# Optimization experiments

Measured on AMD Instinct MI355X. Metric: run time of the kernel, lower is better.

Reference implementation:

```python
import jax, jax.numpy as jnp
import numpy as np

N_NODES, N_GRAPHS, PER_GRAPH, N_EDGES = 20000, 200, 100, 320000
X_DIM, E_DIM, G_DIM = 32, 16, 32
NUM_EMB, HEADS, LAYERS = 64, 2, 3
EPS_GEN, EPS_LN = 1e-7, 1e-5


def _w(k, shape, scale=0.05):
    return (jax.random.normal(k, shape) * scale).astype(jnp.float32)


def _mlp3(x, W1, b1, W2, b2, W3, b3):
    h = jax.nn.leaky_relu(x @ W1 + b1)
    h = jax.nn.leaky_relu(h @ W2 + b2)
    return h @ W3 + b3


def _seg_sum(x, idx, n):
    return jax.ops.segment_sum(x, idx, num_segments=n)


def _seg_mean(x, idx, n):
    s = _seg_sum(x, idx, n)
    cnt = _seg_sum(jnp.ones((x.shape[0],), x.dtype), idx, n)
    return s / jnp.clip(cnt, 1.0, None)[:, None]


def _seg_softmax(logits, idx, n):
    # PyG softmax: subtract per-segment max, normalize with +1e-16
    m = jax.ops.segment_max(logits, idx, num_segments=n)
    m = jnp.where(jnp.isfinite(m), m, 0.0)
    e = jnp.exp(logits - m[idx])
    s = jax.ops.segment_sum(e, idx, num_segments=n)
    return e / (s[idx] + 1e-16)


def _graph_layernorm(x, batch, n_graphs):
    # PyG LayerNorm(mode='graph', affine=False): mean/var over all node-feature
    # entries of each graph.
    f = x.shape[-1]
    cnt = _seg_sum(jnp.ones((x.shape[0],), x.dtype), batch, n_graphs)
    norm = jnp.clip(cnt, 1.0, None) * f
    mean = _seg_sum(x.sum(-1), batch, n_graphs) / norm
    xc = x - mean[batch][:, None]
    var = _seg_sum((xc * xc).sum(-1), batch, n_graphs) / norm
    return xc / jnp.sqrt(var + EPS_LN)[batch][:, None]


def _forward(x, edge_attr, cond, edge_index, batch,
             x2h_W1, x2h_b1, x2h_W2, x2h_b2, x2h_W3, x2h_b3,
             e2h_W1, e2h_b1, e2h_W2, e2h_b2, e2h_W3, e2h_b3,
             c2h_W1, c2h_b1, c2h_W2, c2h_b2, c2h_W3, c2h_b3,
             gen_W, tr_Wq, tr_bq, tr_Wk, tr_bk, tr_Wv, tr_bv, tr_We, tr_Ws, tr_bs,
             lin_W, lin_b, ff_W1, ff_b1, ff_W2, ff_b2):
    N = x.shape[0]
    G = cond.shape[0]
    Naug = N + G
    o = _mlp3(x, x2h_W1, x2h_b1, x2h_W2, x2h_b2, x2h_W3, x2h_b3)
    e = _mlp3(edge_attr, e2h_W1, e2h_b1, e2h_W2, e2h_b2, e2h_W3, e2h_b3)
    c = _mlp3(cond, c2h_W1, c2h_b1, c2h_W2, c2h_b2, c2h_W3, c2h_b3)
    # virtual-node edges: node<->virtual node of its graph (virtual ids = N..N+G-1)
    u = jnp.arange(N, dtype=edge_index.dtype)
    v = batch.astype(edge_index.dtype) + N
    aug_ei = jnp.concatenate([edge_index, jnp.stack([u, v]), jnp.stack([v, u])], axis=1)
    e_p = jnp.zeros((2 * N, NUM_EMB), o.dtype).at[:, 0].set(1.0)
    aug_e = jnp.concatenate([e, e_p], axis=0)
    # add_self_loops(fill_value='mean'): self-loop attr = mean of incoming edge attrs
    loop_attr = _seg_mean(aug_e, aug_ei[1], Naug)
    loops = jnp.arange(Naug, dtype=edge_index.dtype)
    aug_ei = jnp.concatenate([aug_ei, jnp.stack([loops, loops])], axis=1)
    aug_e = jnp.concatenate([aug_e, loop_attr], axis=0)
    aug_batch = jnp.concatenate([batch, jnp.arange(G, dtype=batch.dtype)])
    o = jnp.concatenate([o, c], axis=0)  # [Naug, emb]
    src, dst = aug_ei[0], aug_ei[1]
    scale = 1.0 / float(np.sqrt(NUM_EMB))
    for i in range(LAYERS):
        # GENConv(aggr='add', norm=None, num_layers=1): sum(relu(x_j+e)+eps) + x, then Linear
        msg = jax.nn.relu(o[src] + aug_e) + EPS_GEN
        agg = (_seg_sum(msg, dst, Naug) + o) @ gen_W[i]
        # TransformerConv(2*emb -> emb, heads, edge_dim=emb, concat=True)
        xin = jnp.concatenate([o, agg], axis=1)  # [Naug, 2*emb]
        q = (xin @ tr_Wq[i] + tr_bq[i]).reshape(Naug, HEADS, NUM_EMB)
        k = (xin @ tr_Wk[i] + tr_bk[i]).reshape(Naug, HEADS, NUM_EMB)
        vv = (xin @ tr_Wv[i] + tr_bv[i]).reshape(Naug, HEADS, NUM_EMB)
        eh = (aug_e @ tr_We[i]).reshape(-1, HEADS, NUM_EMB)  # [E, H, C]
        kj = k[src] + eh
        alpha = _seg_softmax(jnp.einsum('ehc,ehc->eh', q[dst], kj) * scale, dst, Naug)
        tout = _seg_sum((vv[src] + eh) * alpha[..., None], dst, Naug)
        tout = tout.reshape(Naug, HEADS * NUM_EMB) + xin @ tr_Ws[i] + tr_bs[i]
        # residual + graph LayerNorm, then FFN + graph LayerNorm
        o = _graph_layernorm(o + tout @ lin_W[i] + lin_b[i], aug_batch, G)
        ff = jax.nn.leaky_relu(o @ ff_W1[i] + ff_b1[i]) @ ff_W2[i] + ff_b2[i]
        o = _graph_layernorm(o + ff, aug_batch, G)
    node_o, virt = o[:N], o[N:]
    glob = jnp.concatenate([_seg_mean(node_o, batch, G), virt, c], axis=1)
    o_final = jnp.concatenate([node_o, c[batch]], axis=1)
    return (o_final, glob)


def setup_inputs() -> dict:
    key = jax.random.key(0)
    ks = iter(jax.random.split(key, 64))
    inp = {}
    inp['x'] = jax.random.normal(next(ks), (N_NODES, X_DIM), dtype=jnp.float32)
    inp['edge_attr'] = jax.random.normal(next(ks), (N_EDGES, E_DIM), dtype=jnp.float32)
    inp['cond'] = jax.random.normal(next(ks), (N_GRAPHS, G_DIM), dtype=jnp.float32)
    src = jax.random.randint(next(ks), (N_EDGES,), 0, N_NODES)
    dst = (src // PER_GRAPH) * PER_GRAPH + jax.random.randint(next(ks), (N_EDGES,), 0, PER_GRAPH)
    inp['edge_index'] = jnp.stack([src, dst]).astype(jnp.int32)
    inp['batch'] = jnp.repeat(jnp.arange(N_GRAPHS, dtype=jnp.int32), PER_GRAPH)
    for p, nin in [('x2h', X_DIM), ('e2h', E_DIM), ('c2h', G_DIM)]:
        inp[p + '_W1'] = _w(next(ks), (nin, NUM_EMB)); inp[p + '_b1'] = _w(next(ks), (NUM_EMB,))
        inp[p + '_W2'] = _w(next(ks), (NUM_EMB, NUM_EMB)); inp[p + '_b2'] = _w(next(ks), (NUM_EMB,))
        inp[p + '_W3'] = _w(next(ks), (NUM_EMB, NUM_EMB)); inp[p + '_b3'] = _w(next(ks), (NUM_EMB,))
    HC = HEADS * NUM_EMB
    inp['gen_W'] = _w(next(ks), (LAYERS, NUM_EMB, NUM_EMB))
    inp['tr_Wq'] = _w(next(ks), (LAYERS, 2 * NUM_EMB, HC)); inp['tr_bq'] = _w(next(ks), (LAYERS, HC))
    inp['tr_Wk'] = _w(next(ks), (LAYERS, 2 * NUM_EMB, HC)); inp['tr_bk'] = _w(next(ks), (LAYERS, HC))
    inp['tr_Wv'] = _w(next(ks), (LAYERS, 2 * NUM_EMB, HC)); inp['tr_bv'] = _w(next(ks), (LAYERS, HC))
    inp['tr_We'] = _w(next(ks), (LAYERS, NUM_EMB, HC))
    inp['tr_Ws'] = _w(next(ks), (LAYERS, 2 * NUM_EMB, HC)); inp['tr_bs'] = _w(next(ks), (LAYERS, HC))
    inp['lin_W'] = _w(next(ks), (LAYERS, HC, NUM_EMB)); inp['lin_b'] = _w(next(ks), (LAYERS, NUM_EMB))
    inp['ff_W1'] = _w(next(ks), (LAYERS, NUM_EMB, 4 * NUM_EMB)); inp['ff_b1'] = _w(next(ks), (LAYERS, 4 * NUM_EMB))
    inp['ff_W2'] = _w(next(ks), (LAYERS, 4 * NUM_EMB, NUM_EMB)); inp['ff_b2'] = _w(next(ks), (LAYERS, NUM_EMB))
    return inp


def reference(x, edge_attr, cond, edge_index, batch,
              x2h_W1, x2h_b1, x2h_W2, x2h_b2, x2h_W3, x2h_b3,
              e2h_W1, e2h_b1, e2h_W2, e2h_b2, e2h_W3, e2h_b3,
              c2h_W1, c2h_b1, c2h_W2, c2h_b2, c2h_W3, c2h_b3,
              gen_W, tr_Wq, tr_bq, tr_Wk, tr_bk, tr_Wv, tr_bv, tr_We, tr_Ws, tr_bs,
              lin_W, lin_b, ff_W1, ff_b1, ff_W2, ff_b2):
    return _forward(x, edge_attr, cond, edge_index, batch,
                    x2h_W1, x2h_b1, x2h_W2, x2h_b2, x2h_W3, x2h_b3,
                    e2h_W1, e2h_b1, e2h_W2, e2h_b2, e2h_W3, e2h_b3,
                    c2h_W1, c2h_b1, c2h_W2, c2h_b2, c2h_W3, c2h_b3,
                    gen_W, tr_Wq, tr_bq, tr_Wk, tr_bk, tr_Wv, tr_bv, tr_We, tr_Ws, tr_bs,
                    lin_W, lin_b, ff_W1, ff_b1, ff_W2, ff_b2)
```

## Files before the change

kernel.cpp:

```cpp
#include <hip/hip_runtime.h>
#include <cstddef>

#define NN   20000
#define NG   200
#define NE   320000
#define NAUG 20200
#define NE2  360000
#define EAUG 380200
#define DD   64
#define HC   128

typedef float  f32x4 __attribute__((ext_vector_type(4)));
typedef short  s16x8 __attribute__((ext_vector_type(8)));

static __device__ __forceinline__ unsigned short bf16r(float f){
  unsigned u = __float_as_uint(f);
  u += 0x7FFFu + ((u >> 16) & 1u);
  return (unsigned short)(u >> 16);
}
static __device__ __forceinline__ float d4(float4 a, float4 b){
  return a.x*b.x + a.y*b.y + a.z*b.z + a.w*b.w;
}
static __device__ __forceinline__ float4 f4ab(float4 a, float s, float4 b, float t){
  return make_float4(a.x*s + b.x*t, a.y*s + b.y*t, a.z*s + b.z*t, a.w*s + b.w*t);
}
static __device__ __forceinline__ float4 f4s(float4 a, float s){
  return make_float4(a.x*s, a.y*s, a.z*s, a.w*s);
}

#define WTAB_INIT { \
  {0,0,128,128,136,128,0},{0,0,128,128,136,128,16384},{0,0,128,128,136,128,32768}, \
  {1,0,128,128,136,128,0},{1,0,128,128,136,128,16384},{1,0,128,128,136,128,32768}, \
  {2,0,128,128,136,128,0},{2,0,128,128,136,128,16384},{2,0,128,128,136,128,32768}, \
  {3,0,128,128,136,128,0},{3,0,128,128,136,128,16384},{3,0,128,128,136,128,32768}, \
  {4,0,64,64,72,64,0},{4,0,64,64,72,64,4096},{4,0,64,64,72,64,8192}, \
  {5,0,128,64,136,64,0},{5,0,128,64,136,64,8192},{5,0,128,64,136,64,16384}, \
  {6,0,64,256,72,256,0},{6,0,64,256,72,256,16384},{6,0,64,256,72,256,32768}, \
  {7,0,256,64,264,64,0},{7,0,256,64,264,64,16384},{7,0,256,64,264,64,32768}, \
  {8,1,64,64,72,128,0},{8,1,64,64,72,128,64},{8,1,64,64,72,128,8192},{8,1,64,64,72,128,8256},{8,1,64,64,72,128,16384},{8,1,64,64,72,128,16448}, \
  {8,0,64,64,72,128,0},{8,0,64,64,72,128,64},{8,0,64,64,72,128,8192},{8,0,64,64,72,128,8256},{8,0,64,64,72,128,16384},{8,0,64,64,72,128,16448}, \
  {9,0,32,64,40,64,0},{10,0,64,64,72,64,0},{11,0,64,64,72,64,0}, \
  {12,0,16,64,40,64,0},{13,0,64,64,72,64,0},{14,0,64,64,72,64,0}, \
  {15,0,32,64,40,64,0},{16,0,64,64,72,64,0},{17,0,64,64,72,64,0} }

static const int WTAB_H[45][7] = WTAB_INIT;
__device__ static const int WTAB_D[45][7] = WTAB_INIT;

struct WPtrs { const float* p[18]; };

__global__ void wconv_all_k(WPtrs wp, unsigned short* __restrict__ outbase){
  int b = blockIdx.x;
  int acc = 0; unsigned ooff = 0;
  #pragma unroll 1
  for (int j = 0; j < 45; j++){
    int e  = WTAB_D[j][3] * WTAB_D[j][4];
    int nb = (e + 255) >> 8;
    if (b < acc + nb){
      int idx = (b - acc)*256 + threadIdx.x;
      if (idx < e){
        int KP = WTAB_D[j][4];
        int n = idx / KP, k = idx % KP;
        float v = 0.f;
        if (k < WTAB_D[j][2]){
          const float* s = wp.p[WTAB_D[j][0]];
          int st = WTAB_D[j][5], so = WTAB_D[j][6];
          v = (WTAB_D[j][1] == 0) ? s[(size_t)so + (size_t)k*st + n]
                                  : s[(size_t)so + (size_t)n*st + k];
        }
        outbase[ooff + idx] = bf16r(v);
      }
      return;
    }
    acc += nb; ooff += (unsigned)e;
  }
}

template<int NT>
__launch_bounds__(256)
__global__ void gemm_mfma_k(const float* __restrict__ A, const float* __restrict__ A2,
                            int M, int K, int lda,
                            const unsigned short* __restrict__ WtG,
                            const float* __restrict__ bias, int act,
                            const float* __restrict__ res, const float* __restrict__ res2,
                            int rstride, float* __restrict__ out, int ostride){
  extern __shared__ unsigned short smem[];
  const int KC  = (K > 128) ? 128 : K;
  const int KPc = KC + 8;
  const int KP  = K + 8;
  unsigned short* Wts  = smem;
  unsigned short* Asub = smem + NT*KPc;
  const int tid = threadIdx.x;
  const int wid = tid >> 6, lane = tid & 63;
  const int lrow = lane & 15, quad = lane >> 4;
  const int m0 = blockIdx.x * 64;
  f32x4 acc[NT/16];
  #pragma unroll
  for (int t = 0; t < NT/16; t++) acc[t] = (f32x4){0.f,0.f,0.f,0.f};

  for (int k0 = 0; k0 < K; k0 += KC){
    const int wv = NT*KPc/8, wrow = KPc/8;
    for (int i = tid; i < wv; i += 256){
      int n = i / wrow, c8 = i % wrow;
      *(uint4*)&Wts[n*KPc + c8*8] = *(const uint4*)&WtG[(size_t)n*KP + k0 + c8*8];
    }
    const int av = 64*KC/4, arow = KC/4;
    for (int i = tid; i < av; i += 256){
      int r = i / arow, c4i = i % arow;
      int m = m0 + r, k = k0 + c4i*4;
      float4 v = make_float4(0.f,0.f,0.f,0.f);
      if (m < M){
        v = *(const float4*)(A + (size_t)m*lda + k);
        if (A2){ float4 w = *(const float4*)(A2 + (size_t)m*lda + k);
                 v.x += w.x; v.y += w.y; v.z += w.z; v.w += w.w; }
      }
      ushort4 s; s.x = bf16r(v.x); s.y = bf16r(v.y); s.z = bf16r(v.z); s.w = bf16r(v.w);
      *(ushort4*)&Asub[r*KPc + c4i*4] = s;
    }
    __syncthreads();
    const int ksteps = KC >> 5;
    for (int ks = 0; ks < ksteps; ks++){
      s16x8 a = *(const s16x8*)&Asub[(wid*16 + lrow)*KPc + ks*32 + quad*8];
      #pragma unroll
      for (int nt = 0; nt < NT/16; nt++){
        s16x8 b = *(const s16x8*)&Wts[(nt*16 + lrow)*KPc + ks*32 + quad*8];
        acc[nt] = __builtin_amdgcn_mfma_f32_16x16x32_bf16(a, b, acc[nt], 0, 0, 0);
      }
    }
    __syncthreads();
  }

  const int mb = m0 + wid*16 + quad*4;
  #pragma unroll
  for (int nt = 0; nt < NT/16; nt++){
    int n = nt*16 + lrow;
    #pragma unroll
    for (int r = 0; r < 4; r++){
      int m = mb + r;
      if (m < M){
        float v = acc[nt][r];
        if (bias) v += bias[n];
        if (act)  v = v > 0.f ? v : 0.01f*v;
        if (res)  v += res [(size_t)m*rstride + n];
        if (res2) v += res2[(size_t)m*rstride + n];
        out[(size_t)m*ostride + n] = v;
      }
    }
  }
}

struct PW4 { const unsigned short* w[4]; const float* b[4]; };

__launch_bounds__(256)
__global__ void qkvs4_k(const float* __restrict__ A, int M, PW4 pw,
                        float* __restrict__ out){
  __shared__ __align__(16) unsigned short Wts[128*136];
  __shared__ __align__(16) unsigned short Asub[64*136];
  const unsigned short* WtG = pw.w[blockIdx.y];
  const float* bias = pw.b[blockIdx.y];
  const int tid = threadIdx.x;
  const int wid = tid >> 6, lane = tid & 63;
  const int lrow = lane & 15, quad = lane >> 4;
  const int m0 = blockIdx.x * 64;
  for (int i = tid; i < 128*17; i += 256){
    int n = i/17, c8 = i%17;
    *(uint4*)&Wts[n*136 + c8*8] = *(const uint4*)&WtG[(size_t)n*136 + c8*8];
  }
  for (int i = tid; i < 64*32; i += 256){
    int r = i >> 5, c4 = (i & 31)*4;
    int m = m0 + r;
    float4 v = make_float4(0.f,0.f,0.f,0.f);
    if (m < M) v = *(const float4*)(A + (size_t)m*128 + c4);
    ushort4 s; s.x=bf16r(v.x); s.y=bf16r(v.y); s.z=bf16r(v.z); s.w=bf16r(v.w);
    *(ushort4*)&Asub[r*136 + c4] = s;
  }
  __syncthreads();
  f32x4 acc[8];
  #pragma unroll
  for (int t=0;t<8;t++) acc[t] = (f32x4){0.f,0.f,0.f,0.f};
  #pragma unroll
  for (int ks = 0; ks < 4; ks++){
    s16x8 a = *(const s16x8*)&Asub[(wid*16 + lrow)*136 + ks*32 + quad*8];
    #pragma unroll
    for (int nt = 0; nt < 8; nt++){
      s16x8 b = *(const s16x8*)&Wts[(nt*16 + lrow)*136 + ks*32 + quad*8];
      acc[nt] = __builtin_amdgcn_mfma_f32_16x16x32_bf16(a, b, acc[nt], 0, 0, 0);
    }
  }
  const int mb = m0 + wid*16 + quad*4;
  const int yoff = blockIdx.y*128;
  #pragma unroll
  for (int nt = 0; nt < 8; nt++){
    int n = nt*16 + lrow;
    #pragma unroll
    for (int r = 0; r < 4; r++){
      int m = mb + r;
      if (m < M) out[(size_t)m*512 + yoff + n] = acc[nt][r] + bias[n];
    }
  }
}

struct PW2 { const unsigned short* w[2]; };

__launch_bounds__(256)
__global__ void qe2_k(const float* __restrict__ qkvs, int M, PW2 pw,
                      float* __restrict__ qe){
  __shared__ __align__(16) unsigned short Wts[64*72];
  __shared__ __align__(16) unsigned short Asub[64*72];
  const unsigned short* WtG = pw.w[blockIdx.y];
  const int tid = threadIdx.x;
  const int wid = tid >> 6, lane = tid & 63;
  const int lrow = lane & 15, quad = lane >> 4;
  const int m0 = blockIdx.x * 64;
  const int yoff = blockIdx.y * 64;
  for (int i = tid; i < 64*9; i += 256){
    int n = i/9, c8 = i%9;
    *(uint4*)&Wts[n*72 + c8*8] = *(const uint4*)&WtG[(size_t)n*72 + c8*8];
  }
  for (int i = tid; i < 64*16; i += 256){
    int r = i >> 4, c4 = (i & 15)*4;
    int m = m0 + r;
    float4 v = make_float4(0.f,0.f,0.f,0.f);
    if (m < M) v = *(const float4*)(qkvs + (size_t)m*512 + yoff + c4);
    ushort4 s; s.x=bf16r(v.x); s.y=bf16r(v.y); s.z=bf16r(v.z); s.w=bf16r(v.w);
    *(ushort4*)&Asub[r*72 + c4] = s;
  }
  __syncthreads();
  f32x4 acc[4];
  #pragma unroll
  for (int t=0;t<4;t++) acc[t] = (f32x4){0.f,0.f,0.f,0.f};
  #pragma unroll
  for (int ks = 0; ks < 2; ks++){
    s16x8 a = *(const s16x8*)&Asub[(wid*16 + lrow)*72 + ks*32 + quad*8];
    #pragma unroll
    for (int nt = 0; nt < 4; nt++){
      s16x8 b = *(const s16x8*)&Wts[(nt*16 + lrow)*72 + ks*32 + quad*8];
      acc[nt] = __builtin_amdgcn_mfma_f32_16x16x32_bf16(a, b, acc[nt], 0, 0, 0);
    }
  }
  const int mb = m0 + wid*16 + quad*4;
  #pragma unroll
  for (int nt = 0; nt < 4; nt++){
    int n = nt*16 + lrow;
    #pragma unroll
    for (int r = 0; r < 4; r++){
      int m = mb + r;
      if (m < M) qe[(size_t)m*HC + yoff + n] = acc[nt][r];
    }
  }
}

__launch_bounds__(256)
__global__ void tout2_k(const float* __restrict__ wv, int M, PW2 pw,
                        const float* __restrict__ t1, const float* __restrict__ qkvs,
                        float* __restrict__ tout){
  __shared__ __align__(16) unsigned short Wts[64*72];
  __shared__ __align__(16) unsigned short Asub[64*72];
  const unsigned short* WtG = pw.w[blockIdx.y];
  const int tid = threadIdx.x;
  const int wid = tid >> 6, lane = tid & 63;
  const int lrow = lane & 15, quad = lane >> 4;
  const int m0 = blockIdx.x * 64;
  const int yoff = blockIdx.y * 64;
  for (int i = tid; i < 64*9; i += 256){
    int n = i/9, c8 = i%9;
    *(uint4*)&Wts[n*72 + c8*8] = *(const uint4*)&WtG[(size_t)n*72 + c8*8];
  }
  for (int i = tid; i < 64*16; i += 256){
    int r = i >> 4, c4 = (i & 15)*4;
    int m = m0 + r;
    float4 v = make_float4(0.f,0.f,0.f,0.f);
    if (m < M) v = *(const float4*)(wv + (size_t)m*HC + yoff + c4);
    ushort4 s; s.x=bf16r(v.x); s.y=bf16r(v.y); s.z=bf16r(v.z); s.w=bf16r(v.w);
    *(ushort4*)&Asub[r*72 + c4] = s;
  }
  __syncthreads();
  f32x4 acc[4];
  #pragma unroll
  for (int t=0;t<4;t++) acc[t] = (f32x4){0.f,0.f,0.f,0.f};
  #pragma unroll
  for (int ks = 0; ks < 2; ks++){
    s16x8 a = *(const s16x8*)&Asub[(wid*16 + lrow)*72 + ks*32 + quad*8];
    #pragma unroll
    for (int nt = 0; nt < 4; nt++){
      s16x8 b = *(const s16x8*)&Wts[(nt*16 + lrow)*72 + ks*32 + quad*8];
      acc[nt] = __builtin_amdgcn_mfma_f32_16x16x32_bf16(a, b, acc[nt], 0, 0, 0);
    }
  }
  const int mb = m0 + wid*16 + quad*4;
  #pragma unroll
  for (int nt = 0; nt < 4; nt++){
    int n = nt*16 + lrow;
    #pragma unroll
    for (int r = 0; r < 4; r++){
      int m = mb + r;
      if (m < M)
        tout[(size_t)m*HC + yoff + n] = acc[nt][r]
          + t1[(size_t)m*HC + yoff + n] + qkvs[(size_t)m*512 + 384 + yoff + n];
    }
  }
}

__launch_bounds__(256)
__global__ void mlp3_mfma_k(const float* __restrict__ X, int M, int Din,
                            const unsigned short* __restrict__ w1t,
                            const unsigned short* __restrict__ w2t,
                            const unsigned short* __restrict__ w3t,
                            const float* __restrict__ b1, const float* __restrict__ b2,
                            const float* __restrict__ b3, float* __restrict__ out){
  __shared__ __align__(16) unsigned short W1s[64*40], W2s[64*72], W3s[64*72];
  __shared__ __align__(16) unsigned short xs[64*40], hs[64*72];
  __shared__ float bsh[192];
  const int tid = threadIdx.x;
  for (int i = tid; i < 320; i += 256)  *(uint4*)&W1s[i*8] = *(const uint4*)&w1t[i*8];
  for (int i = tid; i < 576; i += 256){ *(uint4*)&W2s[i*8] = *(const uint4*)&w2t[i*8];
                                        *(uint4*)&W3s[i*8] = *(const uint4*)&w3t[i*8]; }
  if (tid < 64){ bsh[tid] = b1[tid]; bsh[64+tid] = b2[tid]; bsh[128+tid] = b3[tid]; }
  const int m0 = blockIdx.x * 64;
  for (int i = tid; i < 512; i += 256){
    int r = i >> 3, c4 = (i & 7) * 4;
    int m = m0 + r;
    float4 v = make_float4(0.f,0.f,0.f,0.f);
    if (m < M && c4 < Din) v = *(const float4*)(X + (size_t)m*Din + c4);
    ushort4 s; s.x = bf16r(v.x); s.y = bf16r(v.y); s.z = bf16r(v.z); s.w = bf16r(v.w);
    *(ushort4*)&xs[r*40 + c4] = s;
  }
  __syncthreads();
  const int wid = tid >> 6, lane = tid & 63;
  const int lrow = lane & 15, quad = lane >> 4;
  f32x4 acc[4];

  #pragma unroll
  for (int t = 0; t < 4; t++) acc[t] = (f32x4){0.f,0.f,0.f,0.f};
  {
    s16x8 a = *(const s16x8*)&xs[(wid*16 + lrow)*40 + quad*8];
    #pragma unroll
    for (int nt = 0; nt < 4; nt++){
      s16x8 b = *(const s16x8*)&W1s[(nt*16 + lrow)*40 + quad*8];
      acc[nt] = __builtin_amdgcn_mfma_f32_16x16x32_bf16(a, b, acc[nt], 0, 0, 0);
    }
  }
  #pragma unroll
  for (int nt = 0; nt < 4; nt++){
    int n = nt*16 + lrow;
    #pragma unroll
    for (int r = 0; r < 4; r++){
      float v = acc[nt][r] + bsh[n];
      v = v > 0.f ? v : 0.01f*v;
      hs[(wid*16 + quad*4 + r)*72 + n] = bf16r(v);
    }
  }
  __syncthreads();

  #pragma unroll
  for (int t = 0; t < 4; t++) acc[t] = (f32x4){0.f,0.f,0.f,0.f};
  #pragma unroll
  for (int ks = 0; ks < 2; ks++){
    s16x8 a = *(const s16x8*)&hs[(wid*16 + lrow)*72 + ks*32 + quad*8];
    #pragma unroll
    for (int nt = 0; nt < 4; nt++){
      s16x8 b = *(const s16x8*)&W2s[(nt*16 + lrow)*72 + ks*32 + quad*8];
      acc[nt] = __builtin_amdgcn_mfma_f32_16x16x32_bf16(a, b, acc[nt], 0, 0, 0);
    }
  }
  __syncthreads();
  #pragma unroll
  for (int nt = 0; nt < 4; nt++){
    int n = nt*16 + lrow;
    #pragma unroll
    for (int r = 0; r < 4; r++){
      float v = acc[nt][r] + bsh[64 + n];
      v = v > 0.f ? v : 0.01f*v;
      hs[(wid*16 + quad*4 + r)*72 + n] = bf16r(v);
    }
  }
  __syncthreads();

  #pragma unroll
  for (int t = 0; t < 4; t++) acc[t] = (f32x4){0.f,0.f,0.f,0.f};
  #pragma unroll
  for (int ks = 0; ks < 2; ks++){
    s16x8 a = *(const s16x8*)&hs[(wid*16 + lrow)*72 + ks*32 + quad*8];
    #pragma unroll
    for (int nt = 0; nt < 4; nt++){
      s16x8 b = *(const s16x8*)&W3s[(nt*16 + lrow)*72 + ks*32 + quad*8];
      acc[nt] = __builtin_amdgcn_mfma_f32_16x16x32_bf16(a, b, acc[nt], 0, 0, 0);
    }
  }
  #pragma unroll
  for (int nt = 0; nt < 4; nt++){
    int n = nt*16 + lrow;
    #pragma unroll
    for (int r = 0; r < 4; r++){
      int m = m0 + wid*16 + quad*4 + r;
      if (m < M) out[(size_t)m*64 + n] = acc[nt][r] + bsh[128 + n];
    }
  }
}

__global__ void build_edges_k(const int* __restrict__ ei, const int* __restrict__ batch,
                              int* __restrict__ srcA, int* __restrict__ dstA){
  int idx = blockIdx.x*256 + threadIdx.x;
  if (idx >= EAUG) return;
  int s, d;
  if (idx < NE)          { s = ei[idx];              d = ei[NE+idx]; }
  else if (idx < NE+NN)  { int i = idx-NE;           s = i;            d = batch[i]+NN; }
  else if (idx < NE2)    { int i = idx-(NE+NN);      s = batch[i]+NN;  d = i; }
  else                   { int i = idx-NE2;          s = i;            d = i; }
  srcA[idx]=s; dstA[idx]=d;
}

__global__ void count_k(const int* __restrict__ dstA, int* __restrict__ cnt){
  int e = blockIdx.x*256 + threadIdx.x;
  if (e < EAUG) atomicAdd(&cnt[dstA[e]], 1);
}

__global__ void scan_k(const int* __restrict__ cnt, int* __restrict__ rowptr){
  __shared__ int part[1024];
  int tid = threadIdx.x;
  const int per = (NAUG + 1023) / 1024;
  int base = tid * per;
  int s = 0;
  for (int i=0;i<per;i++){ int idx=base+i; if (idx<NAUG) s += cnt[idx]; }
  part[tid] = s;
  __syncthreads();
  for (int off=1; off<1024; off<<=1){
    int v = (tid>=off) ? part[tid-off] : 0;
    __syncthreads();
    part[tid] += v;
    __syncthreads();
  }
  int run = (tid==0) ? 0 : part[tid-1];
  for (int i=0;i<per;i++){
    int idx=base+i;
    if (idx<NAUG){ rowptr[idx]=run; run += cnt[idx]; }
  }
  if (tid==0) rowptr[NAUG] = EAUG;
}

__global__ void scatter_k(const int* __restrict__ srcA, const int* __restrict__ dstA,
                          const int* __restrict__ rowptr, int* __restrict__ cursor,
                          int* __restrict__ eid, int* __restrict__ esrc){
  int e = blockIdx.x*256 + threadIdx.x;
  if (e >= EAUG) return;
  int d = dstA[e];
  int pos = rowptr[d] + atomicAdd(&cursor[d], 1);
  eid[pos]  = e;
  esrc[pos] = srcA[e];
}

__global__ void set_ep_k(float* __restrict__ aug_e){
  int idx = blockIdx.x*256 + threadIdx.x;
  if (idx >= 2*NN*DD) return;
  int c = idx & 63;
  aug_e[(size_t)NE*DD + idx] = (c==0) ? 1.f : 0.f;
}

__launch_bounds__(256)
__global__ void loopmean_k(const int* __restrict__ rowptr, const int* __restrict__ eid,
                           float* __restrict__ aug_e){
  int tid = threadIdx.x;
  int d = blockIdx.x*16 + (tid>>4);
  if (d >= NAUG) return;
  int t4 = (tid & 15)*4;
  int beg = rowptr[d], end = rowptr[d+1];
  float4 s = make_float4(0.f,0.f,0.f,0.f); int n = 0;
  for (int p=beg; p<end; p++){
    int e = eid[p];
    if (e < NE2){
      float4 a = *(const float4*)(aug_e + (size_t)e*DD + t4);
      s.x += a.x; s.y += a.y; s.z += a.z; s.w += a.w;
      n++;
    }
  }
  float cv = (n < 1) ? 1.f : (float)n;
  *(float4*)(aug_e + (size_t)(NE2+d)*DD + t4) = f4s(s, 1.f/cv);
}

__launch_bounds__(256)
__global__ void msg_csr_k(const float* __restrict__ o, const float* __restrict__ aug_e,
                          const int* __restrict__ rowptr, const int* __restrict__ eid,
                          const int* __restrict__ esrc, float* __restrict__ aggsum){
  int tid = threadIdx.x;
  int d = blockIdx.x*16 + (tid>>4);
  if (d >= NAUG) return;
  int t4 = (tid & 15)*4;
  int beg = rowptr[d], end = rowptr[d+1];
  float4 acc = make_float4(0.f,0.f,0.f,0.f);
  for (int p=beg; p<end; p++){
    int e = eid[p], s = esrc[p];
    float4 ov = *(const float4*)(o + (size_t)s*DD + t4);
    float4 ae = *(const float4*)(aug_e + (size_t)e*DD + t4);
    acc.x += fmaxf(ov.x+ae.x, 0.f) + 1e-7f;
    acc.y += fmaxf(ov.y+ae.y, 0.f) + 1e-7f;
    acc.z += fmaxf(ov.z+ae.z, 0.f) + 1e-7f;
    acc.w += fmaxf(ov.w+ae.w, 0.f) + 1e-7f;
  }
  *(float4*)(aggsum + (size_t)d*DD + t4) = acc;
}

__global__ void copy_o_xin_k(const float* __restrict__ o, float* __restrict__ xin){
  int idx = blockIdx.x*256 + threadIdx.x;
  if (idx >= NAUG*DD) return;
  int n = idx >> 6, c = idx & 63;
  xin[(size_t)n*HC + c] = o[idx];
}

__launch_bounds__(256)
__global__ void attn_k(const float* __restrict__ qkvs, const float* __restrict__ qe,
                       const float* __restrict__ aug_e,
                       const int* __restrict__ rowptr, const int* __restrict__ eid,
                       const int* __restrict__ esrc,
                       float* __restrict__ t1, float* __restrict__ wbuf){
  int tid = threadIdx.x;
  int d = blockIdx.x*16 + (tid>>4);
  if (d >= NAUG) return;
  int t4 = (tid & 15)*4;
  const float* qr = qkvs + (size_t)d*512;
  float4 q0  = *(const float4*)(qr + t4);
  float4 q1  = *(const float4*)(qr + 64 + t4);
  float4 qe0 = *(const float4*)(qe + (size_t)d*HC + t4);
  float4 qe1 = *(const float4*)(qe + (size_t)d*HC + 64 + t4);
  float m0=-1e30f, m1=-1e30f, l0=0.f, l1=0.f;
  float4 a0 = make_float4(0.f,0.f,0.f,0.f), a1 = a0, w0 = a0, w1 = a0;
  int beg = rowptr[d], end = rowptr[d+1];
  for (int p=beg; p<end; p++){
    int e = eid[p], s = esrc[p];
    const float* kr = qkvs + (size_t)s*512;
    float4 k0 = *(const float4*)(kr + 128 + t4);
    float4 k1 = *(const float4*)(kr + 192 + t4);
    float4 v0 = *(const float4*)(kr + 256 + t4);
    float4 v1 = *(const float4*)(kr + 320 + t4);
    float4 ae = *(const float4*)(aug_e + (size_t)e*DD + t4);
    float p0 = d4(q0,k0) + d4(qe0,ae);
    float p1 = d4(q1,k1) + d4(qe1,ae);
    p0 += __shfl_xor(p0,8); p0 += __shfl_xor(p0,4); p0 += __shfl_xor(p0,2); p0 += __shfl_xor(p0,1);
    p1 += __shfl_xor(p1,8); p1 += __shfl_xor(p1,4); p1 += __shfl_xor(p1,2); p1 += __shfl_xor(p1,1);
    p0 *= 0.125f; p1 *= 0.125f;
    float nm0 = fmaxf(m0, p0);
    float sc0 = __expf(m0 - nm0);
    float e0  = __expf(p0 - nm0);
    l0 = l0*sc0 + e0; a0 = f4ab(a0, sc0, v0, e0); w0 = f4ab(w0, sc0, ae, e0); m0 = nm0;
    float nm1 = fmaxf(m1, p1);
    float sc1 = __expf(m1 - nm1);
    float e1  = __expf(p1 - nm1);
    l1 = l1*sc1 + e1; a1 = f4ab(a1, sc1, v1, e1); w1 = f4ab(w1, sc1, ae, e1); m1 = nm1;
  }
  float i0 = 1.f/(l0 + 1e-16f), i1 = 1.f/(l1 + 1e-16f);
  *(float4*)(t1   + (size_t)d*HC + t4)      = f4s(a0, i0);
  *(float4*)(t1   + (size_t)d*HC + 64 + t4) = f4s(a1, i1);
  *(float4*)(wbuf + (size_t)d*HC + t4)      = f4s(w0, i0);
  *(float4*)(wbuf + (size_t)d*HC + 64 + t4) = f4s(w1, i1);
}

__global__ void ln_k(const float* __restrict__ y, float* __restrict__ o){
  int g = blockIdx.x, tid = threadIdx.x;
  float sum=0.f, ss=0.f;
  for (int i=tid; i<101*64; i+=256){
    int nd=i>>6, c=i&63;
    int row = (nd<100) ? g*100+nd : NN+g;
    float v = y[(size_t)row*DD + c];
    sum += v; ss += v*v;
  }
  #pragma unroll
  for (int off=32; off; off>>=1){ sum += __shfl_xor(sum, off); ss += __shfl_xor(ss, off); }
  __shared__ float s1[4], s2[4];
  if ((tid&63)==0){ s1[tid>>6]=sum; s2[tid>>6]=ss; }
  __syncthreads();
  sum = s1[0]+s1[1]+s1[2]+s1[3];
  ss  = s2[0]+s2[1]+s2[2]+s2[3];
  const float inv = 1.f/6464.f;
  float mean = sum*inv;
  float var  = ss*inv - mean*mean;
  float rstd = rsqrtf(var + 1e-5f);
  for (int i=tid; i<101*64; i+=256){
    int nd=i>>6, c=i&63;
    int row = (nd<100) ? g*100+nd : NN+g;
    o[(size_t)row*DD + c] = (y[(size_t)row*DD + c] - mean)*rstd;
  }
}

__global__ void copy_c_o_k(const float* __restrict__ c_emb, float* __restrict__ o){
  int idx = blockIdx.x*256 + threadIdx.x;
  if (idx >= NG*DD) return;
  o[(size_t)NN*DD + idx] = c_emb[idx];
}

__global__ void glob_k(const float* __restrict__ o, const float* __restrict__ c_emb,
                       float* __restrict__ gout){
  int g = blockIdx.x, c = threadIdx.x;
  float acc = 0.f;
  for (int t=0;t<100;t++) acc += o[(size_t)(g*100+t)*DD + c];
  gout[(size_t)g*192 + c]       = acc / 100.f;
  gout[(size_t)g*192 + 64 + c]  = o[(size_t)(NN+g)*DD + c];
  gout[(size_t)g*192 + 128 + c] = c_emb[(size_t)g*DD + c];
}
__global__ void ofinal_k(const float* __restrict__ o, const float* __restrict__ c_emb,
                         const int* __restrict__ batch, float* __restrict__ out){
  int idx = blockIdx.x*256 + threadIdx.x;
  if (idx >= NN*HC) return;
  int n = idx>>7, j = idx&127;
  out[idx] = (j<64) ? o[(size_t)n*DD + j] : c_emb[(size_t)batch[n]*DD + (j-64)];
}

static inline int cdiv(int a, int b){ return (a+b-1)/b; }

static inline void gemm_mfma(int N, const float* A, const float* A2, int M, int K, int lda,
                             const unsigned short* Wt, const float* bias, int act,
                             const float* res, const float* res2, int rstride,
                             float* out, int ostride, hipStream_t st){
  int KC = (K > 128) ? 128 : K;
  int KPc = KC + 8;
  size_t sh = (size_t)(N*KPc + 64*KPc) * 2;
  int grid = cdiv(M, 64);
  if (N == 64)
    gemm_mfma_k<64><<<grid,256,sh,st>>>(A,A2,M,K,lda,Wt,bias,act,res,res2,rstride,out,ostride);
  else if (N == 128)
    gemm_mfma_k<128><<<grid,256,sh,st>>>(A,A2,M,K,lda,Wt,bias,act,res,res2,rstride,out,ostride);
  else
    gemm_mfma_k<256><<<grid,256,sh,st>>>(A,A2,M,K,lda,Wt,bias,act,res,res2,rstride,out,ostride);
}

extern "C" void kernel_launch(void* const* d_in, const int* in_sizes, int n_in,
                              void* d_out, int out_size, void* d_ws, size_t ws_size,
                              hipStream_t stream){
  (void)in_sizes; (void)n_in; (void)out_size;
  const float* x         = (const float*)d_in[0];
  const float* edge_attr = (const float*)d_in[1];
  const float* cond      = (const float*)d_in[2];
  const int*   edge_index= (const int*)  d_in[3];
  const int*   batch     = (const int*)  d_in[4];
  const float* xW1=(const float*)d_in[5],  *xb1=(const float*)d_in[6],
             * xW2=(const float*)d_in[7],  *xb2=(const float*)d_in[8],
             * xW3=(const float*)d_in[9],  *xb3=(const float*)d_in[10];
  const float* eW1=(const float*)d_in[11], *eb1=(const float*)d_in[12],
             * eW2=(const float*)d_in[13], *eb2=(const float*)d_in[14],
             * eW3=(const float*)d_in[15], *eb3=(const float*)d_in[16];
  const float* cW1=(const float*)d_in[17], *cb1=(const float*)d_in[18],
             * cW2=(const float*)d_in[19], *cb2=(const float*)d_in[20],
             * cW3=(const float*)d_in[21], *cb3=(const float*)d_in[22];
  const float* gen_W=(const float*)d_in[23];
  const float* trWq=(const float*)d_in[24], *trbq=(const float*)d_in[25];
  const float* trWk=(const float*)d_in[26], *trbk=(const float*)d_in[27];
  const float* trWv=(const float*)d_in[28], *trbv=(const float*)d_in[29];
  const float* trWe=(const float*)d_in[30];
  const float* trWs=(const float*)d_in[31], *trbs=(const float*)d_in[32];
  const float* linW=(const float*)d_in[33], *linb=(const float*)d_in[34];
  const float* ffW1=(const float*)d_in[35], *ffb1=(const float*)d_in[36];
  const float* ffW2=(const float*)d_in[37], *ffb2=(const float*)d_in[38];
  float* out = (float*)d_out;

  float* ws = (float*)d_ws;
  size_t off = 0;
  auto alloc = [&](size_t n)->float*{ float* p = ws + off; off += (n + 63) & ~(size_t)63; return p; };
  int*      srcA  = (int*)alloc(EAUG);
  int*      dstA  = (int*)alloc(EAUG);
  int*      cnt   = (int*)alloc(NAUG);
  int*      rowptr= (int*)alloc(NAUG+1);
  int*      cursor= (int*)alloc(NAUG);
  int*      eid   = (int*)alloc(EAUG);
  int*      esrc  = (int*)alloc(EAUG);
  float*    aug_e = alloc((size_t)EAUG*DD);
  float*    o     = alloc((size_t)NAUG*DD);
  float*    c_emb = alloc((size_t)NG*DD);
  float*    ybuf  = alloc((size_t)NAUG*DD);
  float*    aggsum= alloc((size_t)NAUG*DD);
  float*    xin   = alloc((size_t)NAUG*HC);
  float*    xqkvs = alloc((size_t)NAUG*512);
  float*    qeb   = alloc((size_t)NAUG*HC);
  float*    toutb = alloc((size_t)NAUG*HC);
  float*    t1    = alloc((size_t)NAUG*HC);
  float*    wbuf  = alloc((size_t)NAUG*HC);
  float*    ffh   = alloc((size_t)NAUG*256);
  unsigned short* warena = (unsigned short*)alloc(222720);
  if (off*sizeof(float) > ws_size) return;

  const unsigned short* wptr[45];
  int wblk = 0;
  { size_t woff = 0;
    for (int j = 0; j < 45; j++){
      wptr[j] = warena + woff;
      int e = WTAB_H[j][3]*WTAB_H[j][4];
      woff += (size_t)e;
      wblk += cdiv(e, 256);
    } }

  WPtrs wp;
  wp.p[0]=trWq; wp.p[1]=trWk; wp.p[2]=trWv; wp.p[3]=trWs; wp.p[4]=gen_W;
  wp.p[5]=linW; wp.p[6]=ffW1; wp.p[7]=ffW2; wp.p[8]=trWe;
  wp.p[9]=xW1; wp.p[10]=xW2; wp.p[11]=xW3;
  wp.p[12]=eW1; wp.p[13]=eW2; wp.p[14]=eW3;
  wp.p[15]=cW1; wp.p[16]=cW2; wp.p[17]=cW3;
  wconv_all_k<<<wblk,256,0,stream>>>(wp, warena);

  build_edges_k<<<cdiv(EAUG,256),256,0,stream>>>(edge_index, batch, srcA, dstA);
  hipMemsetAsync(cnt, 0, sizeof(int)*NAUG, stream);
  hipMemsetAsync(cursor, 0, sizeof(int)*NAUG, stream);
  count_k<<<cdiv(EAUG,256),256,0,stream>>>(dstA, cnt);
  scan_k<<<1,1024,0,stream>>>(cnt, rowptr);
  scatter_k<<<cdiv(EAUG,256),256,0,stream>>>(srcA, dstA, rowptr, cursor, eid, esrc);

  mlp3_mfma_k<<<cdiv(NN,64),256,0,stream>>>(x,        NN, 32, wptr[36],wptr[37],wptr[38], xb1,xb2,xb3, o);
  mlp3_mfma_k<<<cdiv(NG,64),256,0,stream>>>(cond,     NG, 32, wptr[42],wptr[43],wptr[44], cb1,cb2,cb3, c_emb);
  mlp3_mfma_k<<<cdiv(NE,64),256,0,stream>>>(edge_attr,NE, 16, wptr[39],wptr[40],wptr[41], eb1,eb2,eb3, aug_e);
  set_ep_k<<<cdiv(2*NN*DD,256),256,0,stream>>>(aug_e);
  loopmean_k<<<cdiv(NAUG,16),256,0,stream>>>(rowptr, eid, aug_e);
  copy_c_o_k<<<cdiv(NG*DD,256),256,0,stream>>>(c_emb, o);

  for (int L=0; L<3; L++){
    const float* lb_i = linb + (size_t)L*DD;
    const float* f1b  = ffb1 + (size_t)L*256;
    const float* f2b  = ffb2 + (size_t)L*DD;
    const unsigned short* genT = wptr[12+L], *linT = wptr[15+L], *ff1T = wptr[18+L], *ff2T = wptr[21+L];
    PW4 pw4; pw4.w[0]=wptr[0+L]; pw4.w[1]=wptr[3+L]; pw4.w[2]=wptr[6+L]; pw4.w[3]=wptr[9+L];
    pw4.b[0]=trbq+(size_t)L*HC; pw4.b[1]=trbk+(size_t)L*HC;
    pw4.b[2]=trbv+(size_t)L*HC; pw4.b[3]=trbs+(size_t)L*HC;
    PW2 pwE; pwE.w[0]=wptr[24+2*L]; pwE.w[1]=wptr[25+2*L];
    PW2 pwT; pwT.w[0]=wptr[30+2*L]; pwT.w[1]=wptr[31+2*L];

    msg_csr_k<<<cdiv(NAUG,16),256,0,stream>>>(o, aug_e, rowptr, eid, esrc, aggsum);
    copy_o_xin_k<<<cdiv(NAUG*DD,256),256,0,stream>>>(o, xin);
    gemm_mfma( 64, aggsum, o, NAUG, 64, 64, genT, nullptr, 0, nullptr, nullptr, 0, xin+64, HC, stream);
    qkvs4_k<<<dim3(cdiv(NAUG,64),4),256,0,stream>>>(xin, NAUG, pw4, xqkvs);
    qe2_k<<<dim3(cdiv(NAUG,64),2),256,0,stream>>>(xqkvs, NAUG, pwE, qeb);
    attn_k<<<cdiv(NAUG,16),256,0,stream>>>(xqkvs, qeb, aug_e, rowptr, eid, esrc, t1, wbuf);
    tout2_k<<<dim3(cdiv(NAUG,64),2),256,0,stream>>>(wbuf, NAUG, pwT, t1, xqkvs, toutb);
    gemm_mfma( 64, toutb, nullptr, NAUG, 128, 128, linT, lb_i, 0, o, nullptr, DD, ybuf, DD, stream);
    ln_k<<<NG,256,0,stream>>>(ybuf, o);
    gemm_mfma(256, o,   nullptr, NAUG,  64,  64, ff1T, f1b, 1, nullptr, nullptr, 0, ffh, 256, stream);
    gemm_mfma( 64, ffh, nullptr, NAUG, 256, 256, ff2T, f2b, 0, o, nullptr, DD, ybuf, DD, stream);
    ln_k<<<NG,256,0,stream>>>(ybuf, o);
  }

  glob_k<<<NG,64,0,stream>>>(o, c_emb, out + (size_t)NN*HC);
  ofinal_k<<<cdiv(NN*HC,256),256,0,stream>>>(o, c_emb, batch, out);
}
```

Measured before the change: 1.444 ms.

## Process message and attention gathers per graph with shared-memory staged node features

Message aggregation and edge attention are rewritten to run one 512-thread block per graph. Each block first copies that graph's 100 nodes plus its virtual node into shared memory: node embeddings in fp32 for the message kernel, and K/V rows as bf16 for the attention kernel. Source-node reads inside the edge loops then hit shared memory instead of scattered global gathers. The cost is only 200 blocks on the GPU, load imbalance from the virtual node's high in-degree, and reduced K/V precision. It also assumes every edge stays within one graph and that graphs occupy contiguous 100-node ranges.

```diff
diff --git a/kernel.cpp b/kernel.cpp
--- a/kernel.cpp
+++ b/kernel.cpp
@@ -17,6 +17,12 @@
   unsigned u = __float_as_uint(f);
   u += 0x7FFFu + ((u >> 16) & 1u);
   return (unsigned short)(u >> 16);
+}
+static __device__ __forceinline__ float4 b2f4(ushort4 u){
+  return make_float4(__uint_as_float((unsigned)u.x << 16),
+                     __uint_as_float((unsigned)u.y << 16),
+                     __uint_as_float((unsigned)u.z << 16),
+                     __uint_as_float((unsigned)u.w << 16));
 }
 static __device__ __forceinline__ float d4(float4 a, float4 b){
   return a.x*b.x + a.y*b.y + a.z*b.z + a.w*b.w;
@@ -476,26 +482,37 @@
   *(float4*)(aug_e + (size_t)(NE2+d)*DD + t4) = f4s(s, 1.f/cv);
 }
 
-__launch_bounds__(256)
-__global__ void msg_csr_k(const float* __restrict__ o, const float* __restrict__ aug_e,
-                          const int* __restrict__ rowptr, const int* __restrict__ eid,
-                          const int* __restrict__ esrc, float* __restrict__ aggsum){
-  int tid = threadIdx.x;
-  int d = blockIdx.x*16 + (tid>>4);
-  if (d >= NAUG) return;
-  int t4 = (tid & 15)*4;
-  int beg = rowptr[d], end = rowptr[d+1];
-  float4 acc = make_float4(0.f,0.f,0.f,0.f);
-  for (int p=beg; p<end; p++){
-    int e = eid[p], s = esrc[p];
-    float4 ov = *(const float4*)(o + (size_t)s*DD + t4);
-    float4 ae = *(const float4*)(aug_e + (size_t)e*DD + t4);
-    acc.x += fmaxf(ov.x+ae.x, 0.f) + 1e-7f;
-    acc.y += fmaxf(ov.y+ae.y, 0.f) + 1e-7f;
-    acc.z += fmaxf(ov.z+ae.z, 0.f) + 1e-7f;
-    acc.w += fmaxf(ov.w+ae.w, 0.f) + 1e-7f;
-  }
-  *(float4*)(aggsum + (size_t)d*DD + t4) = acc;
+__launch_bounds__(512)
+__global__ void msg_graph_k(const float* __restrict__ o, const float* __restrict__ aug_e,
+                            const int* __restrict__ rowptr, const int* __restrict__ eid,
+                            const int* __restrict__ esrc, float* __restrict__ aggsum){
+  __shared__ __align__(16) float OS[101*72];
+  const int g = blockIdx.x;
+  const int tid = threadIdx.x;
+  for (int i = tid; i < 101*16; i += 512){
+    int ln = i >> 4, c4 = (i & 15)*4;
+    int row = (ln < 100) ? g*100 + ln : NN + g;
+    *(float4*)&OS[ln*72 + c4] = *(const float4*)(o + (size_t)row*DD + c4);
+  }
+  __syncthreads();
+  const int gr = tid >> 4;
+  const int t4 = (tid & 15)*4;
+  for (int ld = gr; ld < 101; ld += 32){
+    int d = (ld < 100) ? g*100 + ld : NN + g;
+    int beg = rowptr[d], end = rowptr[d+1];
+    float4 acc = make_float4(0.f,0.f,0.f,0.f);
+    for (int p=beg; p<end; p++){
+      int e = eid[p], s = esrc[p];
+      int ls = (s >= NN) ? 100 : (s - g*100);
+      float4 ov = *(const float4*)&OS[ls*72 + t4];
+      float4 ae = *(const float4*)(aug_e + (size_t)e*DD + t4);
+      acc.x += fmaxf(ov.x+ae.x, 0.f) + 1e-7f;
+      acc.y += fmaxf(ov.y+ae.y, 0.f) + 1e-7f;
+      acc.z += fmaxf(ov.z+ae.z, 0.f) + 1e-7f;
+      acc.w += fmaxf(ov.w+ae.w, 0.f) + 1e-7f;
+    }
+    *(float4*)(aggsum + (size_t)d*DD + t4) = acc;
+  }
 }
 
 __global__ void copy_o_xin_k(const float* __restrict__ o, float* __restrict__ xin){
@@ -505,51 +522,64 @@
   xin[(size_t)n*HC + c] = o[idx];
 }
 
-__launch_bounds__(256)
-__global__ void attn_k(const float* __restrict__ qkvs, const float* __restrict__ qe,
-                       const float* __restrict__ aug_e,
-                       const int* __restrict__ rowptr, const int* __restrict__ eid,
-                       const int* __restrict__ esrc,
-                       float* __restrict__ t1, float* __restrict__ wbuf){
-  int tid = threadIdx.x;
-  int d = blockIdx.x*16 + (tid>>4);
-  if (d >= NAUG) return;
-  int t4 = (tid & 15)*4;
-  const float* qr = qkvs + (size_t)d*512;
-  float4 q0  = *(const float4*)(qr + t4);
-  float4 q1  = *(const float4*)(qr + 64 + t4);
-  float4 qe0 = *(const float4*)(qe + (size_t)d*HC + t4);
-  float4 qe1 = *(const float4*)(qe + (size_t)d*HC + 64 + t4);
-  float m0=-1e30f, m1=-1e30f, l0=0.f, l1=0.f;
-  float4 a0 = make_float4(0.f,0.f,0.f,0.f), a1 = a0, w0 = a0, w1 = a0;
-  int beg = rowptr[d], end = rowptr[d+1];
-  for (int p=beg; p<end; p++){
-    int e = eid[p], s = esrc[p];
-    const float* kr = qkvs + (size_t)s*512;
-    float4 k0 = *(const float4*)(kr + 128 + t4);
-    float4 k1 = *(const float4*)(kr + 192 + t4);
-    float4 v0 = *(const float4*)(kr + 256 + t4);
-    float4 v1 = *(const float4*)(kr + 320 + t4);
-    float4 ae = *(const float4*)(aug_e + (size_t)e*DD + t4);
-    float p0 = d4(q0,k0) + d4(qe0,ae);
-    float p1 = d4(q1,k1) + d4(qe1,ae);
-    p0 += __shfl_xor(p0,8); p0 += __shfl_xor(p0,4); p0 += __shfl_xor(p0,2); p0 += __shfl_xor(p0,1);
-    p1 += __shfl_xor(p1,8); p1 += __shfl_xor(p1,4); p1 += __shfl_xor(p1,2); p1 += __shfl_xor(p1,1);
-    p0 *= 0.125f; p1 *= 0.125f;
-    float nm0 = fmaxf(m0, p0);
-    float sc0 = __expf(m0 - nm0);
-    float e0  = __expf(p0 - nm0);
-    l0 = l0*sc0 + e0; a0 = f4ab(a0, sc0, v0, e0); w0 = f4ab(w0, sc0, ae, e0); m0 = nm0;
-    float nm1 = fmaxf(m1, p1);
-    float sc1 = __expf(m1 - nm1);
-    float e1  = __expf(p1 - nm1);
-    l1 = l1*sc1 + e1; a1 = f4ab(a1, sc1, v1, e1); w1 = f4ab(w1, sc1, ae, e1); m1 = nm1;
-  }
-  float i0 = 1.f/(l0 + 1e-16f), i1 = 1.f/(l1 + 1e-16f);
-  *(float4*)(t1   + (size_t)d*HC + t4)      = f4s(a0, i0);
-  *(float4*)(t1   + (size_t)d*HC + 64 + t4) = f4s(a1, i1);
-  *(float4*)(wbuf + (size_t)d*HC + t4)      = f4s(w0, i0);
-  *(float4*)(wbuf + (size_t)d*HC + 64 + t4) = f4s(w1, i1);
+__launch_bounds__(512)
+__global__ void attn_graph_k(const float* __restrict__ qkvs, const float* __restrict__ qe,
+                             const float* __restrict__ aug_e,
+                             const int* __restrict__ rowptr, const int* __restrict__ eid,
+                             const int* __restrict__ esrc,
+                             float* __restrict__ t1, float* __restrict__ wbuf){
+  __shared__ __align__(16) unsigned short KV[101*264];
+  const int g = blockIdx.x;
+  const int tid = threadIdx.x;
+  for (int i = tid; i < 101*64; i += 512){
+    int ln = i >> 6, c4 = (i & 63)*4;
+    int row = (ln < 100) ? g*100 + ln : NN + g;
+    float4 v = *(const float4*)(qkvs + (size_t)row*512 + 128 + c4);
+    ushort4 s; s.x=bf16r(v.x); s.y=bf16r(v.y); s.z=bf16r(v.z); s.w=bf16r(v.w);
+    *(ushort4*)&KV[ln*264 + c4] = s;
+  }
+  __syncthreads();
+  const int gr = tid >> 4;
+  const int t4 = (tid & 15)*4;
+  for (int ld = gr; ld < 101; ld += 32){
+    int d = (ld < 100) ? g*100 + ld : NN + g;
+    const float* qr = qkvs + (size_t)d*512;
+    float4 q0  = *(const float4*)(qr + t4);
+    float4 q1  = *(const float4*)(qr + 64 + t4);
+    float4 qe0 = *(const float4*)(qe + (size_t)d*HC + t4);
+    float4 qe1 = *(const float4*)(qe + (size_t)d*HC + 64 + t4);
+    float m0=-1e30f, m1=-1e30f, l0=0.f, l1=0.f;
+    float4 a0 = make_float4(0.f,0.f,0.f,0.f), a1 = a0, w0 = a0, w1 = a0;
+    int beg = rowptr[d], end = rowptr[d+1];
+    for (int p=beg; p<end; p++){
+      int e = eid[p], s = esrc[p];
+      int ls = (s >= NN) ? 100 : (s - g*100);
+      const unsigned short* kr = &KV[ls*264];
+      float4 k0 = b2f4(*(const ushort4*)(kr + t4));
+      float4 k1 = b2f4(*(const ushort4*)(kr + 64 + t4));
+      float4 v0 = b2f4(*(const ushort4*)(kr + 128 + t4));
+      float4 v1 = b2f4(*(const ushort4*)(kr + 192 + t4));
+      float4 ae = *(const float4*)(aug_e + (size_t)e*DD + t4);
+      float p0 = d4(q0,k0) + d4(qe0,ae);
+      float p1 = d4(q1,k1) + d4(qe1,ae);
+      p0 += __shfl_xor(p0,8); p0 += __shfl_xor(p0,4); p0 += __shfl_xor(p0,2); p0 += __shfl_xor(p0,1);
+      p1 += __shfl_xor(p1,8); p1 += __shfl_xor(p1,4); p1 += __shfl_xor(p1,2); p1 += __shfl_xor(p1,1);
+      p0 *= 0.125f; p1 *= 0.125f;
+      float nm0 = fmaxf(m0, p0);
+      float sc0 = __expf(m0 - nm0);
+      float e0  = __expf(p0 - nm0);
+      l0 = l0*sc0 + e0; a0 = f4ab(a0, sc0, v0, e0); w0 = f4ab(w0, sc0, ae, e0); m0 = nm0;
+      float nm1 = fmaxf(m1, p1);
+      float sc1 = __expf(m1 - nm1);
+      float e1  = __expf(p1 - nm1);
+      l1 = l1*sc1 + e1; a1 = f4ab(a1, sc1, v1, e1); w1 = f4ab(w1, sc1, ae, e1); m1 = nm1;
+    }
+    float i0 = 1.f/(l0 + 1e-16f), i1 = 1.f/(l1 + 1e-16f);
+    *(float4*)(t1   + (size_t)d*HC + t4)      = f4s(a0, i0);
+    *(float4*)(t1   + (size_t)d*HC + 64 + t4) = f4s(a1, i1);
+    *(float4*)(wbuf + (size_t)d*HC + t4)      = f4s(w0, i0);
+    *(float4*)(wbuf + (size_t)d*HC + 64 + t4) = f4s(w1, i1);
+  }
 }
 
 __global__ void ln_k(const float* __restrict__ y, float* __restrict__ o){
@@ -717,12 +747,12 @@
     PW2 pwE; pwE.w[0]=wptr[24+2*L]; pwE.w[1]=wptr[25+2*L];
     PW2 pwT; pwT.w[0]=wptr[30+2*L]; pwT.w[1]=wptr[31+2*L];
 
-    msg_csr_k<<<cdiv(NAUG,16),256,0,stream>>>(o, aug_e, rowptr, eid, esrc, aggsum);
+    msg_graph_k<<<NG,512,0,stream>>>(o, aug_e, rowptr, eid, esrc, aggsum);
     copy_o_xin_k<<<cdiv(NAUG*DD,256),256,0,stream>>>(o, xin);
     gemm_mfma( 64, aggsum, o, NAUG, 64, 64, genT, nullptr, 0, nullptr, nullptr, 0, xin+64, HC, stream);
     qkvs4_k<<<dim3(cdiv(NAUG,64),4),256,0,stream>>>(xin, NAUG, pw4, xqkvs);
     qe2_k<<<dim3(cdiv(NAUG,64),2),256,0,stream>>>(xqkvs, NAUG, pwE, qeb);
-    attn_k<<<cdiv(NAUG,16),256,0,stream>>>(xqkvs, qeb, aug_e, rowptr, eid, esrc, t1, wbuf);
+    attn_graph_k<<<NG,512,0,stream>>>(xqkvs, qeb, aug_e, rowptr, eid, esrc, t1, wbuf);
     tout2_k<<<dim3(cdiv(NAUG,64),2),256,0,stream>>>(wbuf, NAUG, pwT, t1, xqkvs, toutb);
     gemm_mfma( 64, toutb, nullptr, NAUG, 128, 128, linT, lb_i, 0, o, nullptr, DD, ybuf, DD, stream);
     ln_k<<<NG,256,0,stream>>>(ybuf, o);
```

Measured after the change: 1.466 ms. About the same (+1.5%).
